# Kernel optimization log

Hardware: AMD Instinct MI355X
Metric: run time of the kernel (lower is better)

## Reference

```python
import jax, jax.numpy as jnp
import numpy as np
from jax import lax

CONF_BIT = 8        # mantissa bits for block-floating-point
CONF_GROUP_SIZE = 36  # elements sharing one exponent


def bfp_quantize(x, bits=CONF_BIT, group_size=CONF_GROUP_SIZE):
    """Group-wise block-floating-point quantization (make_groups_tensor).
    Consecutive groups of `group_size` elements of the flattened tensor share
    the exponent of the group's max magnitude; mantissas are rounded to `bits` bits."""
    shape = x.shape
    flat = x.reshape(-1)
    n = flat.shape[0]
    pad = (-n) % group_size
    flat = jnp.pad(flat, (0, pad))
    g = flat.reshape(-1, group_size)
    max_abs = jnp.max(jnp.abs(g), axis=1, keepdims=True)
    # shared exponent = floor(log2(max|x|)); guard zero groups
    exp = jnp.floor(jnp.log2(jnp.where(max_abs > 0, max_abs, 1.0)))
    step = jnp.exp2(exp - (bits - 1))  # quantization step per group
    qmax = 2 ** (bits - 1) - 1
    q = jnp.clip(jnp.round(g / step), -(qmax + 1), qmax) * step
    q = jnp.where(max_abs > 0, q, 0.0)
    return q.reshape(-1)[:n].reshape(shape)


def setup_inputs() -> dict:
    key = jax.random.key(0)
    k1, k2, k3 = jax.random.split(key, 3)
    B, Cin, Cout, H, W, K = 32, 128, 128, 112, 112, 3
    x = jax.random.normal(k1, (B, Cin, H, W), dtype=jnp.float32)
    fan_in = Cin * K * K
    weight = jax.random.normal(k2, (Cout, Cin, K, K), dtype=jnp.float32) / np.sqrt(fan_in)
    bound = 1.0 / np.sqrt(fan_in)
    bias = jax.random.uniform(k3, (Cout,), dtype=jnp.float32, minval=-bound, maxval=bound)
    return {"x": x, "weight": weight, "bias": bias}


def reference(x, weight, bias):
    # BFP-quantize input and weight, then plain conv2d (stride=1, padding=1)
    xq = bfp_quantize(x)
    wq = bfp_quantize(weight)
    out = lax.conv_general_dilated(
        xq, wq,
        window_strides=(1, 1),
        padding=((1, 1), (1, 1)),
        dimension_numbers=("NCHW", "OIHW", "NCHW"),
    )
    return out + bias[None, :, None, None]
```

## Files before the change

kernel.cpp:

```cpp
#include <hip/hip_runtime.h>

typedef __attribute__((ext_vector_type(8))) short short8;
typedef __attribute__((ext_vector_type(4))) float f32x4;

#define NB     32
#define NC     128
#define HW     112
#define PLANE  12544
#define XTOT   51380224
#define NGX    1427229
#define PADW   114
#define PADPLANE 12996
#define XPAD_BYTES 106463232ULL
#define WG_OFF     XPAD_BYTES
#define SE_OFF     (XPAD_BYTES + 294912ULL)

__device__ __forceinline__ void gld_lds16(const void* g, void* l) {
  __builtin_amdgcn_global_load_lds(
      (__attribute__((address_space(1))) unsigned int*)g,
      (__attribute__((address_space(3))) unsigned int*)l, 16, 0, 0);
}

__device__ __forceinline__ float qmax4(float4 v, float m) {
  m = fmaxf(m, fabsf(v.x)); m = fmaxf(m, fabsf(v.y));
  m = fmaxf(m, fabsf(v.z)); m = fmaxf(m, fabsf(v.w));
  return m;
}

__device__ __forceinline__ int bfp_exp(float m) {
  int e = 0;
  if (m > 0.f) {
    e = (int)((__float_as_uint(m) >> 23) & 255) - 127;
    if (e < -100) e = -100;
  }
  return e;
}

__device__ __forceinline__ unsigned short bfp_q(float v, float inv, float st) {
  float qq = fminf(fmaxf(rintf(v * inv), -128.f), 127.f) * st;
  return (unsigned short)(__float_as_uint(qq) >> 16);
}

__global__ __launch_bounds__(256) void quant_step_x(const float* __restrict__ x,
                                                    signed char* __restrict__ se) {
  __shared__ float lds[9216];
  const int t = threadIdx.x;
  const int base = blockIdx.x * 9216;
  const float4* src = (const float4*)(x + base);
  const int rem4 = (XTOT - base) >> 2;
#pragma unroll
  for (int j = 0; j < 9; ++j) {
    int idx = j * 256 + t;
    float4 v = make_float4(0.f, 0.f, 0.f, 0.f);
    if (idx < rem4) v = src[idx];
    ((float4*)lds)[idx] = v;
  }
  __syncthreads();
  int g = blockIdx.x * 256 + t;
  if (g >= NGX) return;
  const float4* p4 = (const float4*)(lds + t * 36);
  float m = 0.f;
#pragma unroll
  for (int j = 0; j < 9; ++j) m = qmax4(p4[j], m);
  se[g] = (signed char)bfp_exp(m);
}

__global__ __launch_bounds__(64) void quant_w_kernel(const float* __restrict__ w,
                                                     unsigned short* __restrict__ wg) {
  int g = blockIdx.x * 64 + threadIdx.x;
  if (g >= 4096) return;
  const float4* p4 = (const float4*)(w + g * 36);
  float4 v[9];
  float m = 0.f;
#pragma unroll
  for (int j = 0; j < 9; ++j) { v[j] = p4[j]; m = qmax4(v[j], m); }
  int e = bfp_exp(m);
  float inv = __uint_as_float((unsigned)(134 - e) << 23);
  float st  = __uint_as_float((unsigned)(120 + e) << 23);
#pragma unroll
  for (int j = 0; j < 9; ++j) {
    float tmp[4] = {v[j].x, v[j].y, v[j].z, v[j].w};
#pragma unroll
    for (int k = 0; k < 4; ++k) {
      int i = j * 4 + k;
      int f = g * 36 + i;
      int co = f / 1152;
      int rem = f % 1152;
      int ci = rem / 9;
      int rs = rem % 9;
      int stp = rs * 4 + (ci >> 5);
      wg[(stp * 128 + co) * 32 + (ci & 31)] = bfp_q(tmp[k], inv, st);
    }
  }
}

#define TSTR 136
__global__ __launch_bounds__(256) void quant_pad_x(const float* __restrict__ x,
                                                   const signed char* __restrict__ se,
                                                   unsigned short* __restrict__ xpad) {
  __shared__ unsigned short tile[32 * TSTR];
  int b = blockIdx.y;
  int p0 = blockIdx.x * 32;
  int t = threadIdx.x;

  int hid = (blockIdx.y * 392 + blockIdx.x) * 256 + t;
  if (hid < NB * 452 * 16) {
    int hb = hid / (452 * 16);
    int r = hid % (452 * 16);
    int pos = r >> 4, cc = r & 15;
    int hp, wp;
    if (pos < 114)      { hp = 0;             wp = pos; }
    else if (pos < 228) { hp = 113;           wp = pos - 114; }
    else if (pos < 340) { hp = pos - 228 + 1; wp = 0; }
    else                { hp = pos - 340 + 1; wp = 113; }
    float4 z = make_float4(0.f, 0.f, 0.f, 0.f);
    *(float4*)&xpad[((size_t)((hb * 114 + hp) * 114 + wp)) * 128 + cc * 8] = z;
  }

  int pq  = (t & 7) * 4;
  int ci0 = (t >> 3) * 4;
  unsigned short q[4][4];
#pragma unroll
  for (int i = 0; i < 4; ++i) {
    int ci = ci0 + i;
    int f = (b * 128 + ci) * PLANE + p0 + pq;
    float4 v = *(const float4*)(x + f);
    float vv[4] = {v.x, v.y, v.z, v.w};
#pragma unroll
    for (int j = 0; j < 4; ++j) {
      int e = se[(f + j) / 36];
      float inv = __uint_as_float((unsigned)(134 - e) << 23);
      float st  = __uint_as_float((unsigned)(120 + e) << 23);
      q[i][j] = bfp_q(vv[j], inv, st);
    }
  }
#pragma unroll
  for (int j = 0; j < 4; ++j)
    *(ushort4*)&tile[(pq + j) * TSTR + ci0] = make_ushort4(q[0][j], q[1][j], q[2][j], q[3][j]);
  __syncthreads();
  int pl = t >> 3;
  int cc = t & 7;
  int p = p0 + pl;
  int h = p / 112, w = p % 112;
  float4 v0 = *(const float4*)&tile[pl * TSTR + cc * 16];
  float4 v1 = *(const float4*)&tile[pl * TSTR + cc * 16 + 8];
  size_t dst = ((size_t)((b * 114 + h + 1) * 114 + (w + 1))) * 128 + cc * 16;
  *(float4*)&xpad[dst]     = v0;
  *(float4*)&xpad[dst + 8] = v1;
}

__global__ __launch_bounds__(256) void conv_mfma(const unsigned short* __restrict__ xpad,
                                                 const unsigned short* __restrict__ wg,
                                                 const float* __restrict__ bias,
                                                 float* __restrict__ out) {
  __shared__ unsigned short smem[16384];
  char* smb = (char*)smem;
  const int t = threadIdx.x;
  const int lane = t & 63, wv = t >> 6;
  const int lane15 = lane & 15, quad = lane >> 4;
  const int wm = wv >> 1, wn = wv & 1;
  const int b = blockIdx.y;
  const int p0 = blockIdx.x * 128;

  int a_src[2], b_src[2];
#pragma unroll
  for (int i = 0; i < 2; ++i) {
    int idx = t + i * 256;
    int row = idx >> 2;
    int c = idx & 3;
    int sw = (row >> 1) & 3;
    a_src[i] = row * 32 + (c ^ sw) * 8;
    int p = p0 + row;
    int h = p / 112, ww = p % 112;
    b_src[i] = ((b * 114 + h) * 114 + ww) * 128 + (c ^ sw) * 8;
  }

  int a_off[4], b_off[4];
#pragma unroll
  for (int f = 0; f < 4; ++f) {
    int row = wm * 64 + f * 16 + lane15;
    a_off[f] = row * 64 + ((quad ^ ((row >> 1) & 3)) * 16);
    int prow = wn * 64 + f * 16 + lane15;
    b_off[f] = 8192 + prow * 64 + ((quad ^ ((prow >> 1) & 3)) * 16);
  }

  f32x4 acc[4][4];
  f32x4 zero = {0.f, 0.f, 0.f, 0.f};
#pragma unroll
  for (int i = 0; i < 4; ++i)
#pragma unroll
    for (int j = 0; j < 4; ++j) acc[i][j] = zero;

  auto stage = [&](int step, char* dst) {
    int rs = step >> 2, cib = step & 3;
    int r = (rs * 11) >> 5;
    int s = rs - r * 3;
    int aofs = step * 4096;
    int bofs = (r * 114 + s) * 128 + cib * 32;
#pragma unroll
    for (int i = 0; i < 2; ++i) {
      gld_lds16(wg + aofs + a_src[i],   dst + wv * 1024 + i * 4096);
      gld_lds16(xpad + b_src[i] + bofs, dst + 8192 + wv * 1024 + i * 4096);
    }
  };

  auto compute = [&](const char* sb) {
    short8 af[4], bf[4];
#pragma unroll
    for (int f = 0; f < 4; ++f) af[f] = *(const short8*)(sb + a_off[f]);
#pragma unroll
    for (int f = 0; f < 4; ++f) bf[f] = *(const short8*)(sb + b_off[f]);
#pragma unroll
    for (int i = 0; i < 4; ++i)
#pragma unroll
      for (int j = 0; j < 4; ++j)
        acc[i][j] = __builtin_amdgcn_mfma_f32_16x16x32_bf16(af[i], bf[j], acc[i][j], 0, 0, 0);
  };

  char* B0 = smb;
  char* B1 = smb + 16384;

  stage(0, B0);
  __syncthreads();
  for (int it = 0; it < 18; ++it) {
    stage(2 * it + 1, B1);
    compute(B0);
    __syncthreads();
    if (it < 17) stage(2 * it + 2, B0);
    compute(B1);
    __syncthreads();
  }

#pragma unroll
  for (int i = 0; i < 4; ++i)
#pragma unroll
    for (int j = 0; j < 4; ++j) {
      int p = p0 + wn * 64 + j * 16 + lane15;
#pragma unroll
      for (int rr = 0; rr < 4; ++rr) {
        int co = wm * 64 + i * 16 + quad * 4 + rr;
        out[(b * 128 + co) * PLANE + p] = acc[i][j][rr] + bias[co];
      }
    }
}

extern "C" void kernel_launch(void* const* d_in, const int* in_sizes, int n_in,
                              void* d_out, int out_size, void* d_ws, size_t ws_size,
                              hipStream_t stream) {
  const float* x    = (const float*)d_in[0];
  const float* w    = (const float*)d_in[1];
  const float* bias = (const float*)d_in[2];
  float* out = (float*)d_out;
  char* ws = (char*)d_ws;
  unsigned short* xpad = (unsigned short*)ws;
  unsigned short* wg   = (unsigned short*)(ws + WG_OFF);
  signed char*    se   = (signed char*)(ws + SE_OFF);

  quant_step_x<<<(NGX + 255) / 256, 256, 0, stream>>>(x, se);
  quant_w_kernel<<<64, 64, 0, stream>>>(w, wg);
  quant_pad_x<<<dim3(392, 32), 256, 0, stream>>>(x, se, xpad);
  conv_mfma<<<dim3(98, 32), 256, 0, stream>>>(xpad, wg, bias, out);
}
```

Before: 553.1 us.

## Triple-buffer conv pipeline, coalesce weight quant, precompute per-channel exponent scales

The conv main loop moves from a double-buffered schedule with full __syncthreads to a three-buffer LDS ring. It waits with s_waitcnt vmcnt(4) plus s_barrier, so two stages of loads stay in flight, and it raises wave priority around the MFMA block. The weight quantizer is rewritten to stage weights in LDS and write the reordered layout coalesced from 16 blocks of 256 threads. quant_pad_x now precomputes each channel's two possible group scales once in LDS instead of doing a byte load and divide per element. The cost is three times the conv LDS footprint, which may lower occupancy, and hand-written waitcnt assumptions that must match the issued load count.

```diff
diff --git a/kernel.cpp b/kernel.cpp
--- a/kernel.cpp
+++ b/kernel.cpp
@@ -41,6 +41,13 @@
   return (unsigned short)(__float_as_uint(qq) >> 16);
 }
 
+__device__ __forceinline__ float mk_inv(int e) {
+  return __uint_as_float((unsigned)(134 - e) << 23);
+}
+__device__ __forceinline__ float mk_st(int e) {
+  return __uint_as_float((unsigned)(120 + e) << 23);
+}
+
 __global__ __launch_bounds__(256) void quant_step_x(const float* __restrict__ x,
                                                     signed char* __restrict__ se) {
   __shared__ float lds[9216];
@@ -65,32 +72,35 @@
   se[g] = (signed char)bfp_exp(m);
 }
 
-__global__ __launch_bounds__(64) void quant_w_kernel(const float* __restrict__ w,
-                                                     unsigned short* __restrict__ wg) {
-  int g = blockIdx.x * 64 + threadIdx.x;
-  if (g >= 4096) return;
-  const float4* p4 = (const float4*)(w + g * 36);
-  float4 v[9];
-  float m = 0.f;
-#pragma unroll
-  for (int j = 0; j < 9; ++j) { v[j] = p4[j]; m = qmax4(v[j], m); }
-  int e = bfp_exp(m);
-  float inv = __uint_as_float((unsigned)(134 - e) << 23);
-  float st  = __uint_as_float((unsigned)(120 + e) << 23);
-#pragma unroll
-  for (int j = 0; j < 9; ++j) {
-    float tmp[4] = {v[j].x, v[j].y, v[j].z, v[j].w};
-#pragma unroll
-    for (int k = 0; k < 4; ++k) {
-      int i = j * 4 + k;
-      int f = g * 36 + i;
-      int co = f / 1152;
-      int rem = f % 1152;
-      int ci = rem / 9;
-      int rs = rem % 9;
-      int stp = rs * 4 + (ci >> 5);
-      wg[(stp * 128 + co) * 32 + (ci & 31)] = bfp_q(tmp[k], inv, st);
-    }
+__global__ __launch_bounds__(256) void quant_w_kernel(const float* __restrict__ w,
+                                                      unsigned short* __restrict__ wg) {
+  __shared__ float wl[9216];
+  __shared__ float wi[256], wsr[256];
+  const int blk = blockIdx.x;
+  const int t = threadIdx.x;
+  const int base = blk * 9216;
+  const float4* src = (const float4*)(w + base);
+#pragma unroll
+  for (int j = 0; j < 9; ++j) ((float4*)wl)[j * 256 + t] = src[j * 256 + t];
+  __syncthreads();
+  {
+    const float4* p4 = (const float4*)(wl + t * 36);
+    float m = 0.f;
+#pragma unroll
+    for (int j = 0; j < 9; ++j) m = qmax4(p4[j], m);
+    int e = bfp_exp(m);
+    wi[t] = mk_inv(e); wsr[t] = mk_st(e);
+  }
+  __syncthreads();
+  const int cloc = t >> 5, cil = t & 31;
+  const int co = blk * 8 + cloc;
+#pragma unroll
+  for (int stp = 0; stp < 36; ++stp) {
+    int cib = stp & 3, rs = stp >> 2;
+    int ci = cib * 32 + cil;
+    int fl = cloc * 1152 + ci * 9 + rs;
+    int g = fl / 36;
+    wg[(stp * 128 + co) * 32 + cil] = bfp_q(wl[fl], wi[g], wsr[g]);
   }
 }
 
@@ -99,6 +109,8 @@
                                                    const signed char* __restrict__ se,
                                                    unsigned short* __restrict__ xpad) {
   __shared__ unsigned short tile[32 * TSTR];
+  __shared__ float4 ist4[128];
+  __shared__ unsigned char roll[128];
   int b = blockIdx.y;
   int p0 = blockIdx.x * 32;
   int t = threadIdx.x;
@@ -117,6 +129,18 @@
     *(float4*)&xpad[((size_t)((hb * 114 + hp) * 114 + wp)) * 128 + cc * 8] = z;
   }
 
+  if (t < 128) {
+    int ci = t;
+    int f0 = (b * 128 + ci) * PLANE + p0;
+    int g = f0 / 36;
+    int rem = f0 - g * 36;
+    roll[ci] = (unsigned char)(36 - rem);
+    int g1 = g + 1; if (g1 > NGX - 1) g1 = NGX - 1;
+    int e0 = se[g], e1 = se[g1];
+    ist4[ci] = make_float4(mk_inv(e0), mk_st(e0), mk_inv(e1), mk_st(e1));
+  }
+  __syncthreads();
+
   int pq  = (t & 7) * 4;
   int ci0 = (t >> 3) * 4;
   unsigned short q[4][4];
@@ -126,11 +150,13 @@
     int f = (b * 128 + ci) * PLANE + p0 + pq;
     float4 v = *(const float4*)(x + f);
     float vv[4] = {v.x, v.y, v.z, v.w};
+    float4 is_ = ist4[ci];
+    int rl = roll[ci];
 #pragma unroll
     for (int j = 0; j < 4; ++j) {
-      int e = se[(f + j) / 36];
-      float inv = __uint_as_float((unsigned)(134 - e) << 23);
-      float st  = __uint_as_float((unsigned)(120 + e) << 23);
+      bool sec = (pq + j) >= rl;
+      float inv = sec ? is_.z : is_.x;
+      float st  = sec ? is_.w : is_.y;
       q[i][j] = bfp_q(vv[j], inv, st);
     }
   }
@@ -149,12 +175,15 @@
   *(float4*)&xpad[dst + 8] = v1;
 }
 
+#define BUFSZ 16384
+#define WB4() asm volatile("s_waitcnt vmcnt(4)\n\ts_barrier" ::: "memory")
+#define WB0() asm volatile("s_waitcnt vmcnt(0)\n\ts_barrier" ::: "memory")
+
 __global__ __launch_bounds__(256) void conv_mfma(const unsigned short* __restrict__ xpad,
                                                  const unsigned short* __restrict__ wg,
                                                  const float* __restrict__ bias,
                                                  float* __restrict__ out) {
-  __shared__ unsigned short smem[16384];
-  char* smb = (char*)smem;
+  __shared__ __align__(16) char smb[3 * BUFSZ];
   const int t = threadIdx.x;
   const int lane = t & 63, wv = t >> 6;
   const int lane15 = lane & 15, quad = lane >> 4;
@@ -210,26 +239,30 @@
     for (int f = 0; f < 4; ++f) af[f] = *(const short8*)(sb + a_off[f]);
 #pragma unroll
     for (int f = 0; f < 4; ++f) bf[f] = *(const short8*)(sb + b_off[f]);
+    __builtin_amdgcn_s_setprio(1);
 #pragma unroll
     for (int i = 0; i < 4; ++i)
 #pragma unroll
       for (int j = 0; j < 4; ++j)
         acc[i][j] = __builtin_amdgcn_mfma_f32_16x16x32_bf16(af[i], bf[j], acc[i][j], 0, 0, 0);
+    __builtin_amdgcn_s_setprio(0);
   };
 
   char* B0 = smb;
-  char* B1 = smb + 16384;
+  char* B1 = smb + BUFSZ;
+  char* B2 = smb + 2 * BUFSZ;
 
   stage(0, B0);
-  __syncthreads();
-  for (int it = 0; it < 18; ++it) {
-    stage(2 * it + 1, B1);
-    compute(B0);
-    __syncthreads();
-    if (it < 17) stage(2 * it + 2, B0);
-    compute(B1);
-    __syncthreads();
-  }
+  stage(1, B1);
+#pragma unroll 1
+  for (int tt = 0; tt < 33; tt += 3) {
+    WB4(); stage(tt + 2, B2); compute(B0);
+    WB4(); stage(tt + 3, B0); compute(B1);
+    WB4(); stage(tt + 4, B1); compute(B2);
+  }
+  WB4(); stage(35, B2); compute(B0);
+  WB4(); compute(B1);
+  WB0(); compute(B2);
 
 #pragma unroll
   for (int i = 0; i < 4; ++i)
@@ -257,7 +290,7 @@
   signed char*    se   = (signed char*)(ws + SE_OFF);
 
   quant_step_x<<<(NGX + 255) / 256, 256, 0, stream>>>(x, se);
-  quant_w_kernel<<<64, 64, 0, stream>>>(w, wg);
+  quant_w_kernel<<<16, 256, 0, stream>>>(w, wg);
   quant_pad_x<<<dim3(392, 32), 256, 0, stream>>>(x, se, xpad);
   conv_mfma<<<dim3(98, 32), 256, 0, stream>>>(xpad, wg, bias, out);
 }
```

Result: faster. 517.7 us (-6.4%).
